# Kernel tuning notes

Measured on AMD Instinct MI355X. Metric: run time of the kernel, lower is better.

## Reference

```python
import jax, jax.numpy as jnp
from jax import lax
import numpy as np

NUM_HEADS = 12


def setup_inputs() -> dict:
    key = jax.random.key(0)
    ks = jax.random.split(key, 7)
    B, H, W, C = 8, 32, 32, 384
    x = jax.random.normal(ks[0], (B, H, W, C), dtype=jnp.float32)
    cls_token = jax.random.normal(ks[1], (B, 1, C), dtype=jnp.float32)
    qkv_w = jax.random.normal(ks[2], (3 * C, C), dtype=jnp.float32) * 0.02
    proj_w = jax.random.normal(ks[3], (C, C), dtype=jnp.float32) * 0.02
    proj_b = jax.random.normal(ks[4], (C,), dtype=jnp.float32) * 0.02
    lepe_w = jax.random.normal(ks[5], (C, 1, 5, 5), dtype=jnp.float32) * 0.02
    lepe_b = jax.random.normal(ks[6], (C,), dtype=jnp.float32) * 0.02
    return {"x": x, "cls_token": cls_token, "qkv_w": qkv_w,
            "proj_w": proj_w, "proj_b": proj_b,
            "lepe_w": lepe_w, "lepe_b": lepe_b}


def reference(x, cls_token, qkv_w, proj_w, proj_b, lepe_w, lepe_b):
    B, H, W, C = x.shape
    nh = NUM_HEADS
    hd = C // nh
    scale = hd ** (-0.5)

    x_seq = x.reshape(B, H * W, C)                      # [B, N, C]
    x_cat = jnp.concatenate([cls_token, x_seq], axis=1)  # [B, N+1, C]
    N1 = x_cat.shape[1]

    qkv = (x_cat @ qkv_w.T).reshape(B, N1, 3, nh, hd)
    qkv = qkv.transpose(2, 0, 3, 1, 4)                  # [3, B, h, N+1, d]
    q, k, v = qkv[0], qkv[1], qkv[2]

    attn = jnp.einsum('bhqd,bhkd->bhqk', q, k) * scale  # [B, h, N+1, N+1]
    attn = jax.nn.softmax(attn, axis=-1)
    out = jnp.einsum('bhqk,bhkd->bhqd', attn, v)        # [B, h, N+1, d]
    out = out.transpose(0, 2, 1, 3).reshape(B, N1, C)
    cls_out, x_out = out[:, :1, :], out[:, 1:, :]

    # LePE: 5x5 depthwise conv over the spatial grid (NCHW, groups=C)
    lepe = lax.conv_general_dilated(
        x.transpose(0, 3, 1, 2), lepe_w,
        window_strides=(1, 1), padding='SAME',
        feature_group_count=C,
        dimension_numbers=('NCHW', 'OIHW', 'NCHW'))
    lepe = lepe + lepe_b[None, :, None, None]
    lepe = lepe.transpose(0, 2, 3, 1).reshape(B, H * W, C)

    x_out = (x_out + lepe) @ proj_w.T + proj_b
    cls_out = cls_out @ proj_w.T + proj_b
    return x_out.reshape(B, H, W, C), cls_out
```

## Files before the change

kernel.cpp:

```cpp
#include <hip/hip_runtime.h>
#include <math.h>

#define NB 8
#define NHH 32
#define NWW 32
#define NC 384
#define NHEAD 12
#define NHD 32
#define NN1 1025
#define NHW 1024
#define NMROWS (NB * NN1)
#define MPAD 8320
#define NPB 1088
#define MP2 (NB * NPB)
#define NMT (MP2 / 64)
#define CST 1152

typedef float f32x4 __attribute__((ext_vector_type(4)));
typedef __bf16 bf16x8 __attribute__((ext_vector_type(8)));
typedef __bf16 bf16x4 __attribute__((ext_vector_type(4)));
typedef short s16x4 __attribute__((ext_vector_type(4)));
typedef __attribute__((address_space(3))) unsigned int lds_u32;
typedef const __attribute__((address_space(1))) unsigned int glb_u32;

static __device__ __forceinline__ bf16x8 as_bf16x8(uint4 u) {
    union { uint4 a; bf16x8 b; } x; x.a = u; return x.b;
}
static __device__ __forceinline__ unsigned short bfbits(__bf16 b) {
    union { __bf16 a; unsigned short s; } u; u.a = b; return u.s;
}
static __device__ __forceinline__ float bf2f(unsigned short s) {
    union { unsigned u; float f; } x; x.u = ((unsigned)s) << 16; return x.f;
}
static __device__ __forceinline__ unsigned pack2(float a, float b) {
    return (unsigned)bfbits((__bf16)a) | ((unsigned)bfbits((__bf16)b) << 16);
}
static __device__ __forceinline__ f32x4 mfma16(bf16x4 a, bf16x4 b, f32x4 c) {
#if __has_builtin(__builtin_amdgcn_mfma_f32_16x16x16_bf16)
    return __builtin_amdgcn_mfma_f32_16x16x16_bf16(a, b, c, 0, 0, 0);
#else
    union { bf16x4 h; s16x4 s; } ua, ub; ua.h = a; ub.h = b;
    return __builtin_amdgcn_mfma_f32_16x16x16bf16_1k(ua.s, ub.s, c, 0, 0, 0);
#endif
}
static __device__ __forceinline__ int xcd_swz(int i, int nwg) {
    int xcd = i & 7, pos = i >> 3;
    int q = nwg >> 3, r = nwg & 7;
    return xcd * q + (xcd < r ? xcd : r) + pos;
}

#define P_N1 835584
#define P_N2 110592
#define P_N3 36864
#define P_N4 9600
#define P_N5 11520
#define P_TOT (P_N1 + P_N2 + P_N3 + P_N4 + P_N5)

__global__ __launch_bounds__(256) void prep_k(
    const float* __restrict__ x, const float* __restrict__ cls,
    const float* __restrict__ qkv_w, const float* __restrict__ proj_w,
    const float* __restrict__ lepe_w,
    __bf16* __restrict__ Ab, __bf16* __restrict__ wqb, __bf16* __restrict__ wpb,
    float* __restrict__ lepeT, __bf16* __restrict__ aob)
{
    int idx = blockIdx.x * 256 + threadIdx.x;
    if (idx >= P_TOT) return;
    if (idx < P_N1) {
        int e0 = idx * 4;
        int mp = e0 / NC, kk = e0 % NC;
        int b = mp / NPB, n = mp % NPB;
        float4 v = make_float4(0.f, 0.f, 0.f, 0.f);
        if (n < NN1) {
            const float* src = (n == 0) ? (cls + (size_t)b * NC + kk)
                                        : (x + ((size_t)(b * NHW + (n - 1))) * NC + kk);
            v = *(const float4*)src;
        }
        uint2 u; u.x = pack2(v.x, v.y); u.y = pack2(v.z, v.w);
        *(uint2*)(Ab + (size_t)mp * NC + kk) = u;
        return;
    }
    idx -= P_N1;
    if (idx < P_N2) {
        int e0 = idx * 4;
        float4 v = *(const float4*)(qkv_w + e0);
        uint2 u; u.x = pack2(v.x, v.y); u.y = pack2(v.z, v.w);
        *(uint2*)(wqb + e0) = u;
        return;
    }
    idx -= P_N2;
    if (idx < P_N3) {
        int e0 = idx * 4;
        float4 v = *(const float4*)(proj_w + e0);
        uint2 u; u.x = pack2(v.x, v.y); u.y = pack2(v.z, v.w);
        *(uint2*)(wpb + e0) = u;
        return;
    }
    idx -= P_N3;
    if (idx < P_N4) {
        int tap = idx / NC, cc = idx % NC;
        lepeT[tap * NC + cc] = lepe_w[cc * 25 + tap];
        return;
    }
    idx -= P_N4;
    {
        uint2 z; z.x = 0; z.y = 0;
        *(uint2*)(aob + (size_t)NMROWS * NC + idx * 4) = z;
    }
}

#define LP 72
#define QSCALE 0.25505654007f
#define CPD 136

union QkvSm {
    struct { __bf16 As[2][64][64]; __bf16 Bs[2][128][64]; } g;
    __bf16 C[64][CPD];
};

__global__ __launch_bounds__(256) void qkv_mfma_k(
    const __bf16* __restrict__ A, const __bf16* __restrict__ W,
    __bf16* __restrict__ Cg)
{
    __shared__ QkvSm sm;
    const int tid  = threadIdx.x;
    const int lane = tid & 63;
    const int wid  = tid >> 6;
    const int wr   = wid >> 1, wc = wid & 1;
    const int c    = lane & 15, hg = lane >> 4;
    const int wg   = xcd_swz(blockIdx.x, 9 * NMT);
    const int tile = wg % 9;
    const int m0   = (wg / 9) * 64;
    const int n0   = tile * 128;

    int aw_row[2], aw_col[2];
#pragma unroll
    for (int j = 0; j < 2; ++j) {
        int word = (wid * 2 + j) * 64 + lane;
        int row = word >> 3, slot = word & 7;
        aw_row[j] = row;
        aw_col[j] = (slot ^ (row & 7)) * 8;
    }
    int bw_row[4], bw_col[4];
#pragma unroll
    for (int j = 0; j < 4; ++j) {
        int word = (wid * 4 + j) * 64 + lane;
        int row = word >> 3, slot = word & 7;
        bw_row[j] = row;
        bw_col[j] = (slot ^ (row & 7)) * 8;
    }

    f32x4 acc[2][4];
#pragma unroll
    for (int i = 0; i < 2; ++i)
#pragma unroll
        for (int j = 0; j < 4; ++j) acc[i][j] = f32x4{0.f, 0.f, 0.f, 0.f};

    __bf16* asbase = &sm.g.As[0][0][0];
    __bf16* bsbase = &sm.g.Bs[0][0][0];

    auto stage = [&](int buf, int k0) {
#pragma unroll
        for (int j = 0; j < 2; ++j) {
            const __bf16* src = A + (size_t)(m0 + aw_row[j]) * NC + k0 + aw_col[j];
            __bf16* dst = asbase + (size_t)buf * 4096 + (wid * 2 + j) * 512;
            __builtin_amdgcn_global_load_lds((glb_u32*)src, (lds_u32*)dst, 16, 0, 0);
        }
#pragma unroll
        for (int j = 0; j < 4; ++j) {
            const __bf16* src = W + (size_t)(n0 + bw_row[j]) * NC + k0 + bw_col[j];
            __bf16* dst = bsbase + (size_t)buf * 8192 + (wid * 4 + j) * 512;
            __builtin_amdgcn_global_load_lds((glb_u32*)src, (lds_u32*)dst, 16, 0, 0);
        }
    };

    stage(0, 0);
    __syncthreads();

    for (int t = 0; t < 6; ++t) {
        const int cur = t & 1;
        if (t < 5) stage(cur ^ 1, (t + 1) * 64);

        const __bf16* ab = asbase + (size_t)cur * 4096;
        const __bf16* bb = bsbase + (size_t)cur * 8192;
#pragma unroll
        for (int ks = 0; ks < 2; ++ks) {
            bf16x8 af[2], bfr[4];
#pragma unroll
            for (int i = 0; i < 2; ++i) {
                int row = wr * 32 + i * 16 + c;
                int slot = (ks * 4 + hg) ^ (row & 7);
                af[i] = as_bf16x8(*(const uint4*)(ab + row * 64 + slot * 8));
            }
#pragma unroll
            for (int j = 0; j < 4; ++j) {
                int row = wc * 64 + j * 16 + c;
                int slot = (ks * 4 + hg) ^ (row & 7);
                bfr[j] = as_bf16x8(*(const uint4*)(bb + row * 64 + slot * 8));
            }
            __builtin_amdgcn_s_setprio(1);
#pragma unroll
            for (int i = 0; i < 2; ++i)
#pragma unroll
                for (int j = 0; j < 4; ++j)
                    acc[i][j] = __builtin_amdgcn_mfma_f32_16x16x32_bf16(
                        af[i], bfr[j], acc[i][j], 0, 0, 0);
            __builtin_amdgcn_s_setprio(0);
        }
        if (t < 5) __syncthreads();
    }

    __syncthreads();
    const float qs = (tile < 3) ? QSCALE : 1.0f;
#pragma unroll
    for (int i = 0; i < 2; ++i)
#pragma unroll
        for (int r = 0; r < 4; ++r) {
            int row = wr * 32 + i * 16 + 4 * hg + r;
#pragma unroll
            for (int j = 0; j < 4; ++j)
                sm.C[row][wc * 64 + j * 16 + c] = (__bf16)(acc[i][j][r] * qs);
        }
    __syncthreads();

#pragma unroll
    for (int it = 0; it < 4; ++it) {
        int idx   = it * 256 + tid;
        int row   = idx >> 4;
        int chunk = idx & 15;
        uint4 u = *(const uint4*)&sm.C[row][chunk * 8];
        *(uint4*)(Cg + (size_t)(m0 + row) * CST + n0 + chunk * 8) = u;
    }
}

__global__ __launch_bounds__(256) void proj_mfma_k(
    const __bf16* __restrict__ A, const __bf16* __restrict__ W,
    const float* __restrict__ bias, float* __restrict__ out)
{
    __shared__ __bf16 As[128][LP];
    __shared__ __bf16 Bs[64][LP];
    const int tid  = threadIdx.x;
    const int lane = tid & 63;
    const int wid  = tid >> 6;
    const int wr   = wid >> 1, wc = wid & 1;
    const int c    = lane & 15, hg = lane >> 4;
    const int wg   = xcd_swz(blockIdx.x, 6 * 65);
    const int m0   = (wg / 6) * 128;
    const int n0   = (wg % 6) * 64;
    const int srow = tid >> 1;
    const int scol = (tid & 1) * 32;
    const int brow = tid >> 2;
    const int bcol = (tid & 3) * 16;

    f32x4 acc[4][2];
#pragma unroll
    for (int i = 0; i < 4; ++i)
#pragma unroll
        for (int j = 0; j < 2; ++j) acc[i][j] = f32x4{0.f, 0.f, 0.f, 0.f};

    uint4 a4[4], b4[2];
#pragma unroll
    for (int s = 0; s < 4; ++s)
        a4[s] = *(const uint4*)(A + (size_t)(m0 + srow) * NC + scol + s * 8);
#pragma unroll
    for (int s = 0; s < 2; ++s)
        b4[s] = *(const uint4*)(W + (size_t)(n0 + brow) * NC + bcol + s * 8);

    for (int k0 = 0; k0 < NC; k0 += 64) {
        __syncthreads();
#pragma unroll
        for (int s = 0; s < 4; ++s) *(uint4*)&As[srow][scol + s * 8] = a4[s];
#pragma unroll
        for (int s = 0; s < 2; ++s) *(uint4*)&Bs[brow][bcol + s * 8] = b4[s];
        __syncthreads();
        if (k0 + 64 < NC) {
#pragma unroll
            for (int s = 0; s < 4; ++s)
                a4[s] = *(const uint4*)(A + (size_t)(m0 + srow) * NC + k0 + 64 + scol + s * 8);
#pragma unroll
            for (int s = 0; s < 2; ++s)
                b4[s] = *(const uint4*)(W + (size_t)(n0 + brow) * NC + k0 + 64 + bcol + s * 8);
        }
#pragma unroll
        for (int ks = 0; ks < 2; ++ks) {
            bf16x8 af[4], bfr[2];
#pragma unroll
            for (int i = 0; i < 4; ++i)
                af[i] = as_bf16x8(*(const uint4*)&As[wr * 64 + i * 16 + c][ks * 32 + hg * 8]);
#pragma unroll
            for (int j = 0; j < 2; ++j)
                bfr[j] = as_bf16x8(*(const uint4*)&Bs[wc * 32 + j * 16 + c][ks * 32 + hg * 8]);
#pragma unroll
            for (int i = 0; i < 4; ++i)
#pragma unroll
                for (int j = 0; j < 2; ++j)
                    acc[i][j] = __builtin_amdgcn_mfma_f32_16x16x32_bf16(
                        af[i], bfr[j], acc[i][j], 0, 0, 0);
        }
    }

#pragma unroll
    for (int i = 0; i < 4; ++i)
#pragma unroll
        for (int r = 0; r < 4; ++r) {
            int m = m0 + wr * 64 + i * 16 + 4 * hg + r;
            if (m >= NMROWS) continue;
            int b = m / NN1, n = m % NN1;
            float* dstrow = (n == 0)
                ? (out + (size_t)NB * NHW * NC + (size_t)b * NC)
                : (out + ((size_t)(b * NHW) + (n - 1)) * NC);
#pragma unroll
            for (int j = 0; j < 2; ++j) {
                int col = n0 + wc * 32 + j * 16 + c;
                dstrow[col] = acc[i][j][r] + bias[col];
            }
        }
}

#define KC 64
#define VPAD 72
#define NCH ((NN1 + KC - 1) / KC)

__global__ __launch_bounds__(256) void attn_mfma_k(
    const __bf16* __restrict__ Cg, __bf16* __restrict__ ao)
{
    __shared__ unsigned short Vs[2][32][VPAD];

    const int wg    = xcd_swz(blockIdx.x, 9 * NB * NHEAD);
    const int qtile = wg % 9;
    const int bh    = wg / 9;
    const int b     = bh / NHEAD;
    const int hh    = bh % NHEAD;
    const int tid   = threadIdx.x;
    const int lane  = tid & 63;
    const int wv    = tid >> 6;
    const int c     = lane & 15;
    const int hg    = lane >> 4;
    const int q0    = qtile * 128 + wv * 32;
    const size_t MBp = (size_t)b * NPB;

    const __bf16* qb = Cg + hh * 32;
    const __bf16* kb = Cg + 384 + hh * 32;
    const __bf16* vb = Cg + 768 + hh * 32;

    uint4 zero4 = make_uint4(0, 0, 0, 0);
    bf16x8 qf[2];
#pragma unroll
    for (int qt = 0; qt < 2; ++qt) {
        int row = q0 + qt * 16 + c;
        uint4 u = (row < NN1)
            ? *(const uint4*)(qb + (MBp + row) * CST + hg * 8) : zero4;
        qf[qt] = as_bf16x8(u);
    }

    f32x4 O[2][2];
#pragma unroll
    for (int qt = 0; qt < 2; ++qt)
#pragma unroll
        for (int dt = 0; dt < 2; ++dt) O[qt][dt] = f32x4{0.f, 0.f, 0.f, 0.f};
    float lrun[2] = {0.f, 0.f};

    const int k_row = tid >> 2;
    const int k_col = (tid & 3) * 8;

    uint4 kcur[4], knxt[4];
#pragma unroll
    for (int kt = 0; kt < 4; ++kt)
        kcur[kt] = *(const uint4*)(kb + (MBp + kt * 16 + c) * CST + hg * 8);
    uint4 vr = *(const uint4*)(vb + (MBp + k_row) * CST + k_col);
    {
        union { uint4 u; unsigned short s[8]; } vu; vu.u = vr;
#pragma unroll
        for (int j = 0; j < 8; ++j) Vs[0][k_col + j][k_row] = vu.s[j];
    }
    __syncthreads();

    for (int t = 0; t < NCH; ++t) {
        const int kt0 = t * KC;
        const int cur = t & 1;
        const bool haveNext = (t + 1 < NCH);
        if (haveNext) {
#pragma unroll
            for (int kt = 0; kt < 4; ++kt)
                knxt[kt] = *(const uint4*)(kb + (MBp + kt0 + KC + kt * 16 + c) * CST + hg * 8);
            vr = *(const uint4*)(vb + (MBp + kt0 + KC + k_row) * CST + k_col);
        }
        const bool full = (kt0 + KC <= NN1);

        bf16x4 pa[2][4];
#pragma unroll
        for (int qt = 0; qt < 2; ++qt) {
            f32x4 Sf[4];
            __builtin_amdgcn_s_setprio(1);
#pragma unroll
            for (int kt = 0; kt < 4; ++kt)
                Sf[kt] = __builtin_amdgcn_mfma_f32_16x16x32_bf16(
                    as_bf16x8(kcur[kt]), qf[qt], f32x4{0.f, 0.f, 0.f, 0.f}, 0, 0, 0);
            __builtin_amdgcn_s_setprio(0);

            if (!full) {
#pragma unroll
                for (int kt = 0; kt < 4; ++kt)
#pragma unroll
                    for (int r = 0; r < 4; ++r) {
                        int key = kt0 + kt * 16 + 4 * hg + r;
                        if (key >= NN1) Sf[kt][r] = -3.0e38f;
                    }
            }
            float psum = 0.f;
#pragma unroll
            for (int kt = 0; kt < 4; ++kt) {
                float p0 = exp2f(Sf[kt][0]);
                float p1 = exp2f(Sf[kt][1]);
                float p2 = exp2f(Sf[kt][2]);
                float p3 = exp2f(Sf[kt][3]);
                psum += (p0 + p1) + (p2 + p3);
                pa[qt][kt] = bf16x4{(__bf16)p0, (__bf16)p1, (__bf16)p2, (__bf16)p3};
            }
            lrun[qt] += psum;
        }

        bf16x4 vbf[2][4];
#pragma unroll
        for (int dt = 0; dt < 2; ++dt)
#pragma unroll
            for (int kt = 0; kt < 4; ++kt)
                vbf[dt][kt] = *(const bf16x4*)&Vs[cur][dt * 16 + c][kt * 16 + 4 * hg];

        __builtin_amdgcn_s_setprio(1);
#pragma unroll
        for (int qt = 0; qt < 2; ++qt)
#pragma unroll
            for (int dt = 0; dt < 2; ++dt)
#pragma unroll
                for (int kt = 0; kt < 4; ++kt)
                    O[qt][dt] = mfma16(pa[qt][kt], vbf[dt][kt], O[qt][dt]);
        __builtin_amdgcn_s_setprio(0);

        if (haveNext) {
            union { uint4 u; unsigned short s[8]; } vu; vu.u = vr;
#pragma unroll
            for (int j = 0; j < 8; ++j) Vs[cur ^ 1][k_col + j][k_row] = vu.s[j];
#pragma unroll
            for (int kt = 0; kt < 4; ++kt) kcur[kt] = knxt[kt];
            __syncthreads();
        }
    }

#pragma unroll
    for (int qt = 0; qt < 2; ++qt) {
        float Ls = lrun[qt];
        Ls += __shfl_xor(Ls, 16);
        Ls += __shfl_xor(Ls, 32);
#pragma unroll
        for (int r = 0; r < 4; ++r) {
            float lr_ = __shfl(Ls, 4 * hg + r);
            int row = q0 + qt * 16 + 4 * hg + r;
            float inv = (lr_ > 0.f) ? 1.0f / lr_ : 0.f;
            if (row < NN1) {
#pragma unroll
                for (int dt = 0; dt < 2; ++dt)
                    ao[((size_t)(b * NN1 + row)) * NC + hh * NHD + dt * 16 + c]
                        = (__bf16)(O[qt][dt][r] * inv);
            }
        }
    }
}

__global__ __launch_bounds__(256) void lepe2_k(
    const float* __restrict__ x, const float* __restrict__ wT,
    const float* __restrict__ bias, __bf16* __restrict__ ao)
{
    int idx = blockIdx.x * 256 + threadIdx.x;
    if (idx >= NB * (NHH / 2) * NWW * (NC / 4)) return;
    int cg = idx % (NC / 4);
    int c4 = cg * 4;
    int pos = idx / (NC / 4);
    int ww = pos % NWW;
    int hp = (pos / NWW) % (NHH / 2);
    int b = pos / (NWW * (NHH / 2));
    int hh = hp * 2;

    float4 bv = *(const float4*)(bias + c4);
    float a0[2], a1[2], a2[2], a3[2];
    a0[0] = bv.x; a1[0] = bv.y; a2[0] = bv.z; a3[0] = bv.w;
    a0[1] = bv.x; a1[1] = bv.y; a2[1] = bv.z; a3[1] = bv.w;

#pragma unroll
    for (int i = 0; i < 6; ++i) {
        int y = hh + i - 2;
        bool yv = (unsigned)y < NHH;
#pragma unroll
        for (int j = 0; j < 5; ++j) {
            int xw = ww + j - 2;
            if (yv && (unsigned)xw < NWW) {
                float4 xv = *(const float4*)(x + (((size_t)b * NHH + y) * NWW + xw) * NC + c4);
                if (i < 5) {
                    float4 wv = *(const float4*)(wT + (i * 5 + j) * NC + c4);
                    a0[0] += xv.x * wv.x; a1[0] += xv.y * wv.y;
                    a2[0] += xv.z * wv.z; a3[0] += xv.w * wv.w;
                }
                if (i >= 1) {
                    float4 wv = *(const float4*)(wT + ((i - 1) * 5 + j) * NC + c4);
                    a0[1] += xv.x * wv.x; a1[1] += xv.y * wv.y;
                    a2[1] += xv.z * wv.z; a3[1] += xv.w * wv.w;
                }
            }
        }
    }

#pragma unroll
    for (int rr = 0; rr < 2; ++rr) {
        size_t m = (size_t)b * NN1 + 1 + (hh + rr) * NWW + ww;
        uint2* aop = (uint2*)(ao + m * NC + c4);
        uint2 old = *aop;
        float r0 = a0[rr] + bf2f((unsigned short)(old.x & 0xffff));
        float r1 = a1[rr] + bf2f((unsigned short)(old.x >> 16));
        float r2 = a2[rr] + bf2f((unsigned short)(old.y & 0xffff));
        float r3 = a3[rr] + bf2f((unsigned short)(old.y >> 16));
        uint2 nw; nw.x = pack2(r0, r1); nw.y = pack2(r2, r3);
        *aop = nw;
    }
}

extern "C" void kernel_launch(void* const* d_in, const int* in_sizes, int n_in,
                              void* d_out, int out_size, void* d_ws, size_t ws_size,
                              hipStream_t stream)
{
    const float* x      = (const float*)d_in[0];
    const float* cls    = (const float*)d_in[1];
    const float* qkv_w  = (const float*)d_in[2];
    const float* proj_w = (const float*)d_in[3];
    const float* proj_b = (const float*)d_in[4];
    const float* lepe_w = (const float*)d_in[5];
    const float* lepe_b = (const float*)d_in[6];
    float* out = (float*)d_out;
    char*  ws  = (char*)d_ws;

    size_t off = 0;
    __bf16* Ab    = (__bf16*)(ws + off); off += (size_t)MP2 * NC * 2;
    __bf16* wqb   = (__bf16*)(ws + off); off += (size_t)1152 * NC * 2;
    __bf16* wpb   = (__bf16*)(ws + off); off += (size_t)NC * NC * 2;
    float*  lepeT = (float*) (ws + off); off += (size_t)25 * NC * 4;
    __bf16* Cg    = (__bf16*)(ws + off); off += (size_t)MP2 * CST * 2;
    __bf16* aob   = (__bf16*)(ws + off); off += (size_t)MPAD * NC * 2;

    {
        prep_k<<<(P_TOT + 255) / 256, 256, 0, stream>>>(
            x, cls, qkv_w, proj_w, lepe_w, Ab, wqb, wpb, lepeT, aob);
    }
    {
        qkv_mfma_k<<<9 * NMT, 256, 0, stream>>>(Ab, wqb, Cg);
    }
    {
        attn_mfma_k<<<9 * NB * NHEAD, 256, 0, stream>>>(Cg, aob);
    }
    {
        int total = NB * (NHW / 2) * (NC / 4);
        lepe2_k<<<(total + 255) / 256, 256, 0, stream>>>(x, lepeT, lepe_b, aob);
    }
    {
        proj_mfma_k<<<6 * 65, 256, 0, stream>>>(aob, wpb, proj_b, out);
    }
}
```

Before: 127.2 us.

## Split attention key range across two workgroups and merge partials in combine kernel

The attention kernel gains a templated split mode in which each (batch, head, q-tile) is processed by two workgroups. Each covers half of the key chunks and writes unnormalised fp32 output partials and row sums to workspace. A new combine kernel adds the two partials, normalises them and writes the bf16 attention output. The goal is to double the number of workgroups and shorten each one's serial key loop so the GPU is better filled. The cost is an extra kernel launch and roughly tens of MB of fp32 partial traffic. The split path runs only when the workspace is large enough, otherwise the original single-pass kernel is used.

New measurement: 135.3 us. 1.06x slower.

```diff
diff --git a/kernel.cpp b/kernel.cpp
--- a/kernel.cpp
+++ b/kernel.cpp
@@ -15,6 +15,8 @@
 #define MP2 (NB * NPB)
 #define NMT (MP2 / 64)
 #define CST 1152
+#define NBH (NB * NHEAD)
+#define QROWS 1152
 
 typedef float f32x4 __attribute__((ext_vector_type(4)));
 typedef __bf16 bf16x8 __attribute__((ext_vector_type(8)));
@@ -320,14 +322,20 @@
 #define VPAD 72
 #define NCH ((NN1 + KC - 1) / KC)
 
+template <int MODE>
 __global__ __launch_bounds__(256) void attn_mfma_k(
-    const __bf16* __restrict__ Cg, __bf16* __restrict__ ao)
+    const __bf16* __restrict__ Cg, __bf16* __restrict__ ao,
+    float* __restrict__ Op, float* __restrict__ lp)
 {
     __shared__ unsigned short Vs[2][32][VPAD];
 
-    const int wg    = xcd_swz(blockIdx.x, 9 * NB * NHEAD);
-    const int qtile = wg % 9;
-    const int bh    = wg / 9;
+    const int nwg   = 9 * NBH * (MODE ? 2 : 1);
+    const int wg    = xcd_swz(blockIdx.x, nwg);
+    int ks, rest;
+    if (MODE) { ks = wg & 1; rest = wg >> 1; }
+    else      { ks = 0;      rest = wg;      }
+    const int qtile = rest % 9;
+    const int bh    = rest / 9;
     const int b     = bh / NHEAD;
     const int hh    = bh % NHEAD;
     const int tid   = threadIdx.x;
@@ -337,6 +345,8 @@
     const int hg    = lane >> 4;
     const int q0    = qtile * 128 + wv * 32;
     const size_t MBp = (size_t)b * NPB;
+    const int c0 = MODE ? (ks ? 9 : 0) : 0;
+    const int c1 = MODE ? (ks ? NCH : 9) : NCH;
 
     const __bf16* qb = Cg + hh * 32;
     const __bf16* kb = Cg + 384 + hh * 32;
@@ -365,8 +375,8 @@
     uint4 kcur[4], knxt[4];
 #pragma unroll
     for (int kt = 0; kt < 4; ++kt)
-        kcur[kt] = *(const uint4*)(kb + (MBp + kt * 16 + c) * CST + hg * 8);
-    uint4 vr = *(const uint4*)(vb + (MBp + k_row) * CST + k_col);
+        kcur[kt] = *(const uint4*)(kb + (MBp + c0 * KC + kt * 16 + c) * CST + hg * 8);
+    uint4 vr = *(const uint4*)(vb + (MBp + c0 * KC + k_row) * CST + k_col);
     {
         union { uint4 u; unsigned short s[8]; } vu; vu.u = vr;
 #pragma unroll
@@ -374,10 +384,10 @@
     }
     __syncthreads();
 
-    for (int t = 0; t < NCH; ++t) {
+    int cur = 0;
+    for (int t = c0; t < c1; ++t, cur ^= 1) {
         const int kt0 = t * KC;
-        const int cur = t & 1;
-        const bool haveNext = (t + 1 < NCH);
+        const bool haveNext = (t + 1 < c1);
         if (haveNext) {
 #pragma unroll
             for (int kt = 0; kt < 4; ++kt)
@@ -446,24 +456,69 @@
         }
     }
 
-#pragma unroll
-    for (int qt = 0; qt < 2; ++qt) {
-        float Ls = lrun[qt];
-        Ls += __shfl_xor(Ls, 16);
-        Ls += __shfl_xor(Ls, 32);
-#pragma unroll
-        for (int r = 0; r < 4; ++r) {
-            float lr_ = __shfl(Ls, 4 * hg + r);
-            int row = q0 + qt * 16 + 4 * hg + r;
-            float inv = (lr_ > 0.f) ? 1.0f / lr_ : 0.f;
-            if (row < NN1) {
-#pragma unroll
-                for (int dt = 0; dt < 2; ++dt)
-                    ao[((size_t)(b * NN1 + row)) * NC + hh * NHD + dt * 16 + c]
-                        = (__bf16)(O[qt][dt][r] * inv);
-            }
-        }
-    }
+    if (MODE) {
+        float* Ob = Op + ((size_t)(ks * NBH + bh)) * QROWS * 32;
+        float* lb = lp + ((size_t)(ks * NBH + bh)) * QROWS;
+#pragma unroll
+        for (int qt = 0; qt < 2; ++qt) {
+            float Ls = lrun[qt];
+            Ls += __shfl_xor(Ls, 16);
+            Ls += __shfl_xor(Ls, 32);
+#pragma unroll
+            for (int r = 0; r < 4; ++r) {
+                float lr_ = __shfl(Ls, 4 * hg + r);
+                int row = q0 + qt * 16 + 4 * hg + r;
+                Ob[(size_t)row * 32 + c]      = O[qt][0][r];
+                Ob[(size_t)row * 32 + 16 + c] = O[qt][1][r];
+                if (c == 0) lb[row] = lr_;
+            }
+        }
+    } else {
+#pragma unroll
+        for (int qt = 0; qt < 2; ++qt) {
+            float Ls = lrun[qt];
+            Ls += __shfl_xor(Ls, 16);
+            Ls += __shfl_xor(Ls, 32);
+#pragma unroll
+            for (int r = 0; r < 4; ++r) {
+                float lr_ = __shfl(Ls, 4 * hg + r);
+                int row = q0 + qt * 16 + 4 * hg + r;
+                float inv = (lr_ > 0.f) ? 1.0f / lr_ : 0.f;
+                if (row < NN1) {
+#pragma unroll
+                    for (int dt = 0; dt < 2; ++dt)
+                        ao[((size_t)(b * NN1 + row)) * NC + hh * NHD + dt * 16 + c]
+                            = (__bf16)(O[qt][dt][r] * inv);
+                }
+            }
+        }
+    }
+}
+
+#define CMB_TOT (NBH * NN1 * 8)
+
+__global__ __launch_bounds__(256) void combine_k(
+    const float* __restrict__ Op, const float* __restrict__ lp,
+    __bf16* __restrict__ ao)
+{
+    int idx = blockIdx.x * 256 + threadIdx.x;
+    if (idx >= CMB_TOT) return;
+    int d4 = idx & 7;
+    int rest = idx >> 3;
+    int n = rest % NN1;
+    int bh = rest / NN1;
+    int b = bh / NHEAD, hh = bh % NHEAD;
+
+    size_t o0 = ((size_t)bh * QROWS + n) * 32 + d4 * 4;
+    size_t o1 = ((size_t)(NBH + bh) * QROWS + n) * 32 + d4 * 4;
+    float4 a = *(const float4*)(Op + o0);
+    float4 bb = *(const float4*)(Op + o1);
+    float l = lp[(size_t)bh * QROWS + n] + lp[(size_t)(NBH + bh) * QROWS + n];
+    float inv = (l > 0.f) ? 1.0f / l : 0.f;
+    float r0 = (a.x + bb.x) * inv, r1 = (a.y + bb.y) * inv;
+    float r2 = (a.z + bb.z) * inv, r3 = (a.w + bb.w) * inv;
+    uint2 w; w.x = pack2(r0, r1); w.y = pack2(r2, r3);
+    *(uint2*)(ao + ((size_t)(b * NN1 + n)) * NC + hh * NHD + d4 * 4) = w;
 }
 
 __global__ __launch_bounds__(256) void lepe2_k(
@@ -543,6 +598,11 @@
     float*  lepeT = (float*) (ws + off); off += (size_t)25 * NC * 4;
     __bf16* Cg    = (__bf16*)(ws + off); off += (size_t)MP2 * CST * 2;
     __bf16* aob   = (__bf16*)(ws + off); off += (size_t)MPAD * NC * 2;
+    float*  Op    = (float*)(ws + off);
+    size_t  opBytes = (size_t)2 * NBH * QROWS * 32 * 4;
+    float*  lp    = (float*)(ws + off + opBytes);
+    size_t  needed = off + opBytes + (size_t)2 * NBH * QROWS * 4;
+    const bool split = (ws_size >= needed);
 
     {
         prep_k<<<(P_TOT + 255) / 256, 256, 0, stream>>>(
@@ -551,8 +611,11 @@
     {
         qkv_mfma_k<<<9 * NMT, 256, 0, stream>>>(Ab, wqb, Cg);
     }
-    {
-        attn_mfma_k<<<9 * NB * NHEAD, 256, 0, stream>>>(Cg, aob);
+    if (split) {
+        attn_mfma_k<1><<<9 * NBH * 2, 256, 0, stream>>>(Cg, aob, Op, lp);
+        combine_k<<<(CMB_TOT + 255) / 256, 256, 0, stream>>>(Op, lp, aob);
+    } else {
+        attn_mfma_k<0><<<9 * NBH, 256, 0, stream>>>(Cg, aob, nullptr, nullptr);
     }
     {
         int total = NB * (NHW / 2) * (NC / 4);
```
